# Optimization experiments

Hardware: AMD Instinct MI355X
Metric: run time of the kernel (lower is better)

## Reference

```python
import jax, jax.numpy as jnp
import numpy as np

B, N, C, PH, PW = 16, 256, 1, 16, 16
G, HID = 8, 256
TEMP = 0.5
EPS = 1e-5


def setup_inputs() -> dict:
    key = jax.random.key(0)
    ks = jax.random.split(key, 16)
    f32 = jnp.float32
    def kaiming(k, shape):  # fan_out mode for convs, OIHW
        fan_out = shape[0] * shape[2] * shape[3]
        return jax.random.normal(k, shape, f32) * np.float32(np.sqrt(2.0 / fan_out))
    def lin(k, shape):  # nn.init.normal_(w, 0, 0.01)
        return jax.random.normal(k, shape, f32) * np.float32(0.01)
    return {
        "x": jax.random.normal(ks[0], (B, N, C, PH, PW), f32),
        "conv1_w": kaiming(ks[1], (32, 1, 3, 3)),  "conv1_b": jnp.zeros((32,), f32),
        "bn1_g": jnp.ones((32,), f32),  "bn1_b": jnp.zeros((32,), f32),
        "conv2_w": kaiming(ks[2], (64, 32, 3, 3)), "conv2_b": jnp.zeros((64,), f32),
        "bn2_g": jnp.ones((64,), f32),  "bn2_b": jnp.zeros((64,), f32),
        "conv3_w": kaiming(ks[3], (128, 64, 3, 3)), "conv3_b": jnp.zeros((128,), f32),
        "bn3_g": jnp.ones((128,), f32), "bn3_b": jnp.zeros((128,), f32),
        "fc_w": lin(ks[4], (HID, 128)),       "fc_b": jnp.zeros((HID,), f32),
        "g1_w": lin(ks[5], (2 * HID, HID)),   "g1_b": jnp.zeros((2 * HID,), f32),
        "ln1_g": jnp.ones((2 * HID,), f32),   "ln1_b": jnp.zeros((2 * HID,), f32),
        "g2_w": lin(ks[6], (2 * HID, 2 * HID)), "g2_b": jnp.zeros((2 * HID,), f32),
        "ln2_g": jnp.ones((2 * HID,), f32),   "ln2_b": jnp.zeros((2 * HID,), f32),
        "g3_w": lin(ks[7], (G, 2 * HID)),     "g3_b": jnp.zeros((G,), f32),
    }


def _conv(h, w, b):
    out = jax.lax.conv_general_dilated(h, w, (1, 1), 'SAME',
        dimension_numbers=('NCHW', 'OIHW', 'NCHW'))
    return out + b[None, :, None, None]


def _bn_train(h, g, b):  # batch stats over (N, H, W), biased variance
    m = h.mean(axis=(0, 2, 3), keepdims=True)
    v = h.var(axis=(0, 2, 3), keepdims=True)
    return (h - m) * jax.lax.rsqrt(v + EPS) * g[None, :, None, None] + b[None, :, None, None]


def _ln(h, g, b):
    m = h.mean(axis=-1, keepdims=True)
    v = h.var(axis=-1, keepdims=True)
    return (h - m) * jax.lax.rsqrt(v + EPS) * g + b


def reference(x, conv1_w, conv1_b, bn1_g, bn1_b, conv2_w, conv2_b, bn2_g, bn2_b,
              conv3_w, conv3_b, bn3_g, bn3_b, fc_w, fc_b,
              g1_w, g1_b, ln1_g, ln1_b, g2_w, g2_b, ln2_g, ln2_b, g3_w, g3_b):
    Bx, Nx, Cx, ph, pw = x.shape
    Gx = g3_w.shape[0]
    K = Nx // Gx  # num_patches_per_group

    # ---- patch encoder (conv + BN(train) + ReLU x3, GAP, Linear) ----
    h = x.reshape(Bx * Nx, Cx, ph, pw)
    h = jax.nn.relu(_bn_train(_conv(h, conv1_w, conv1_b), bn1_g, bn1_b))
    h = jax.nn.relu(_bn_train(_conv(h, conv2_w, conv2_b), bn2_g, bn2_b))
    h = jax.nn.relu(_bn_train(_conv(h, conv3_w, conv3_b), bn3_g, bn3_b))
    feat = h.mean(axis=(2, 3))                     # [B*N, 128] (AdaptiveAvgPool2d(1))
    feat = feat @ fc_w.T + fc_b                    # [B*N, HID]
    feat = feat.reshape(Bx, Nx, -1)

    # ---- grouping network ----
    h = jax.nn.relu(_ln(feat @ g1_w.T + g1_b, ln1_g, ln1_b))
    h = jax.nn.relu(_ln(h @ g2_w.T + g2_b, ln2_g, ln2_b))
    logits = (h @ g3_w.T + g3_b) / TEMP            # [B, N, G]
    assignment = jax.nn.softmax(logits, axis=2)    # [B, N, G]

    # ---- per-group top-K weighted patch gather (training path) ----
    w = jnp.transpose(assignment, (0, 2, 1))       # [B, G, N]
    vals, idx = jax.lax.top_k(w, K)                # [B, G, K] (descending, matches sort)
    idx_e = idx[:, :, :, None, None, None]         # [B, G, K, 1, 1, 1]
    gathered = jnp.take_along_axis(x[:, None], idx_e, axis=2)  # [B, G, K, C, ph, pw]
    output = gathered * vals[:, :, :, None, None, None]
    return output, assignment
```

## Files before the change

kernel.cpp:

```cpp
#include <hip/hip_runtime.h>


#define WS_W1   0
#define WS_B1   288
#define WS_W2   320
#define WS_B2   18752
#define WS_W3   18816
#define WS_B3   92544
#define WS_FCW  92672
#define WS_FCB  125440
#define WS_G1W  125696
#define WS_G1B  256768
#define WS_L1G  257280
#define WS_L1B  257792
#define WS_G2W  258304
#define WS_G2B  520448
#define WS_L2G  520960
#define WS_L2B  521472
#define WS_G3W  521984
#define WS_G3B  526080
#define D_ACC1  263044
#define D_ACC2  (D_ACC1 + 4096)
#define D_ACC3  (D_ACC2 + 8192)
#define D_FEAT  (D_ACC3 + 16384)
#define D_AFF1  (D_FEAT + 524288)
#define D_AFF2  (D_AFF1 + 64)
#define D_AFF3  (D_AFF2 + 128)
#define D_ZN    553408
#define Z2_OFF_B 6532096ull


__global__ __launch_bounds__(256) void k_zero(double* __restrict__ dst){
  int i = blockIdx.x*256 + threadIdx.x;
  if(i < D_ZN) dst[i] = 0.0;
}

struct WP { const float* p[18]; };

__global__ __launch_bounds__(256) void k_cvt(WP wp, float* __restrict__ dst){
  const int segn[18] = {288,32,18432,64,73728,128,32768,256,131072,512,512,512,262144,512,512,512,4096,8};
  const int sego[18] = {WS_W1,WS_B1,WS_W2,WS_B2,WS_W3,WS_B3,WS_FCW,WS_FCB,WS_G1W,WS_G1B,
                        WS_L1G,WS_L1B,WS_G2W,WS_G2B,WS_L2G,WS_L2B,WS_G3W,WS_G3B};
  int s = blockIdx.y;
  int i = blockIdx.x*256 + threadIdx.x;
  if(i < segn[s]){
    if(s == 4){
      int oc = i / 576;
      int rem = i - oc*576;
      int ic = rem / 9;
      int j  = rem - ic*9;
      dst[WS_W3 + ic*1152 + j*128 + oc] = wp.p[4][i];
    } else {
      dst[sego[s]+i] = wp.p[s][i];
    }
  }
}

__global__ __launch_bounds__(64) void k_fin(const double* __restrict__ acc, int C,
                                            const float* __restrict__ gam, const float* __restrict__ bet,
                                            double* __restrict__ aff){
  int c = blockIdx.x, t = threadIdx.x;
  double s = acc[t*2*C + c*2];
  double q = acc[t*2*C + c*2 + 1];
  #pragma unroll
  for(int off=32;off;off>>=1){ s += __shfl_down(s,off); q += __shfl_down(q,off); }
  if(t==0){
    double m = s*(1.0/1048576.0);
    double v = q*(1.0/1048576.0) - m*m;
    double sc = (double)gam[c] / sqrt(v + 1e-5);
    aff[2*c]   = sc;
    aff[2*c+1] = (double)bet[c] - m*sc;
  }
}

__global__ __launch_bounds__(256) void k_p1(const float* __restrict__ x, const float* __restrict__ wf,
                                            double* __restrict__ acc1){
  __shared__ float xp[324];
  __shared__ double red[4][32][2];
  int p = blockIdx.x, t = threadIdx.x;
  for(int i=t;i<324;i+=256) xp[i]=0.f;
  __syncthreads();
  int py=t>>4, px=t&15;
  xp[(py+1)*18 + px + 1] = x[(size_t)p*256+t];
  __syncthreads();
  float nb[9];
  #pragma unroll
  for(int j=0;j<9;j++) nb[j] = xp[(py+j/3)*18 + px + (j%3)];
  int wave=t>>6, lane=t&63;
  for(int c=0;c<32;c++){
    float a = wf[WS_B1+c];
    #pragma unroll
    for(int j=0;j<9;j++) a = fmaf(nb[j], wf[WS_W1+c*9+j], a);
    double av=(double)a;
    double s=av, q=av*av;
    #pragma unroll
    for(int off=32;off;off>>=1){ s+=__shfl_down(s,off); q+=__shfl_down(q,off); }
    if(lane==0){ red[wave][c][0]=s; red[wave][c][1]=q; }
  }
  __syncthreads();
  if(t<64){
    int c=t>>1, st=t&1;
    double v = red[0][c][st]+red[1][c][st]+red[2][c][st]+red[3][c][st];
    atomicAdd(&acc1[(p&63)*64 + c*2 + st], v);
  }
}

__global__ __launch_bounds__(256) void k_p2(const float* __restrict__ x, const float* __restrict__ wf,
                                            const double* __restrict__ aff1, double* __restrict__ acc2,
                                            float* __restrict__ z2, int nS){
  __shared__ float xp[324];
  __shared__ float h1f[32*324];
  int p=blockIdx.x, t=threadIdx.x;
  for(int i=t;i<324;i+=256) xp[i]=0.f;
  for(int i=t;i<32*324;i+=256) h1f[i]=0.f;
  __syncthreads();
  int py=t>>4, px=t&15;
  xp[(py+1)*18 + px + 1] = x[(size_t)p*256+t];
  __syncthreads();
  {
    float nb[9];
    #pragma unroll
    for(int j=0;j<9;j++) nb[j] = xp[(py+j/3)*18 + px + (j%3)];
    for(int c=0;c<32;c++){
      float a = wf[WS_B1+c];
      #pragma unroll
      for(int j=0;j<9;j++) a = fmaf(nb[j], wf[WS_W1+c*9+j], a);
      h1f[c*324 + (py+1)*18 + (px+1)] = fmaxf(fmaf((float)aff1[2*c], a, (float)aff1[2*c+1]), 0.f);
    }
  }
  __syncthreads();
  int col=t&15, og=t>>4;
  bool wr = (p < nS);
  double sT[4]={0,0,0,0}, qT[4]={0,0,0,0};
  #pragma unroll 1
  for(int half=0; half<2; ++half){
    float acc[4][8];
    #pragma unroll
    for(int o=0;o<4;o++){
      float bv = wf[WS_B2 + og*4 + o];
      #pragma unroll
      for(int r=0;r<8;r++) acc[o][r]=bv;
    }
    #pragma unroll 1
    for(int ic=0; ic<32; ++ic){
      const float* wrow = wf + WS_W2 + (og*4*32 + ic)*9;
      #pragma unroll
      for(int j=0;j<9;j++){
        float w4[4];
        #pragma unroll
        for(int o=0;o<4;o++) w4[o] = wrow[o*288 + j];
        int dy=j/3, dx=j%3;
        #pragma unroll
        for(int r=0;r<8;r++){
          float m = h1f[ic*324 + (half*8 + r + dy)*18 + col + dx];
          #pragma unroll
          for(int o=0;o<4;o++) acc[o][r] = fmaf(m, w4[o], acc[o][r]);
        }
      }
    }
    #pragma unroll
    for(int o=0;o<4;o++){
      #pragma unroll
      for(int r=0;r<8;r++){ double v=(double)acc[o][r]; sT[o]+=v; qT[o]+=v*v; }
      if(wr){
        int c = og*4+o;
        #pragma unroll
        for(int r=0;r<8;r++) z2[((size_t)p*64+c)*256 + (half*8+r)*16 + col] = acc[o][r];
      }
    }
  }
  #pragma unroll
  for(int o=0;o<4;o++){
    double s=sT[o], q=qT[o];
    #pragma unroll
    for(int off=8;off;off>>=1){ s+=__shfl_down(s,off,16); q+=__shfl_down(q,off,16); }
    if(col==0){
      int c = og*4+o;
      atomicAdd(&acc2[(p&63)*128 + c*2 + 0], s);
      atomicAdd(&acc2[(p&63)*128 + c*2 + 1], q);
    }
  }
}

__global__ __launch_bounds__(512) void k_cs(const float* __restrict__ wf, const double* __restrict__ aff2,
                                            double* __restrict__ acc3, const float* __restrict__ z2){
  __shared__ float h2S[32*180];
  int bid=blockIdx.x, t=threadIdx.x;
  int p = bid>>1, r0 = (bid&1)*8;
  for(int i=t;i<5760;i+=512) h2S[i]=0.f;
  int col=t&15, og=t>>4;
  float acc[4][8];
  #pragma unroll
  for(int o=0;o<4;o++){
    float bv = wf[WS_B3 + og*4 + o];
    #pragma unroll
    for(int r=0;r<8;r++) acc[o][r]=bv;
  }
  const float* wog = wf + WS_W3 + og*4;
  float4 wc = *reinterpret_cast<const float4*>(wog);
  #pragma unroll 1
  for(int half=0; half<2; ++half){
    __syncthreads();
    for(int i=t;i<5120;i+=512){
      int ch2 = i/160, rem = i - ch2*160;
      int row = rem>>4, c2 = rem&15;
      int gr = r0 - 1 + row;
      if(gr>=0 && gr<16){
        int ch = half*32 + ch2;
        float zv = z2[((size_t)p*64+ch)*256 + gr*16 + c2];
        h2S[ch2*180 + row*18 + c2+1] = fmaxf(fmaf((float)aff2[2*ch], zv, (float)aff2[2*ch+1]), 0.f);
      }
    }
    __syncthreads();
    #pragma unroll 1
    for(int ic2=0; ic2<32; ++ic2){
      int ic = half*32 + ic2;
      float a[10][3];
      #pragma unroll
      for(int lr=0; lr<10; ++lr){
        #pragma unroll
        for(int dx=0; dx<3; ++dx) a[lr][dx] = h2S[ic2*180 + lr*18 + col + dx];
      }
      const float* wp = wog + ic*1152;
      #pragma unroll
      for(int j=0;j<9;j++){
        float4 wn = *reinterpret_cast<const float4*>(wp + (j+1)*128);
        int dy=j/3, dx=j%3;
        float w4[4] = {wc.x, wc.y, wc.z, wc.w};
        #pragma unroll
        for(int o=0;o<4;o++){
          #pragma unroll
          for(int r=0;r<8;r++) acc[o][r] = fmaf(a[r+dy][dx], w4[o], acc[o][r]);
        }
        wc = wn;
      }
    }
  }
  #pragma unroll
  for(int o=0;o<4;o++){
    double s=0.0, q=0.0;
    #pragma unroll
    for(int r=0;r<8;r++){ double v=(double)acc[o][r]; s+=v; q+=v*v; }
    #pragma unroll
    for(int off=8; off; off>>=1){ s += __shfl_down(s, off, 16); q += __shfl_down(q, off, 16); }
    if(col==0){
      int c = og*4+o;
      atomicAdd(&acc3[(bid&63)*256 + c*2 + 0], s);
      atomicAdd(&acc3[(bid&63)*256 + c*2 + 1], q);
    }
  }
}

__global__ __launch_bounds__(512) void k_cf(const float* __restrict__ wf, const double* __restrict__ aff2,
                                            const double* __restrict__ aff3, double* __restrict__ feat,
                                            const float* __restrict__ z2){
  __shared__ float h2S[32*180];
  int bid=blockIdx.x, t=threadIdx.x;
  int p = bid>>1, r0 = (bid&1)*8;
  for(int i=t;i<5760;i+=512) h2S[i]=0.f;
  int col=t&15, og=t>>4;
  float acc[4][8];
  #pragma unroll
  for(int o=0;o<4;o++){
    float bv = wf[WS_B3 + og*4 + o];
    #pragma unroll
    for(int r=0;r<8;r++) acc[o][r]=bv;
  }
  const float* wog = wf + WS_W3 + og*4;
  float4 wc = *reinterpret_cast<const float4*>(wog);
  #pragma unroll 1
  for(int half=0; half<2; ++half){
    __syncthreads();
    for(int i=t;i<5120;i+=512){
      int ch2 = i/160, rem = i - ch2*160;
      int row = rem>>4, c2 = rem&15;
      int gr = r0 - 1 + row;
      if(gr>=0 && gr<16){
        int ch = half*32 + ch2;
        float zv = z2[((size_t)p*64+ch)*256 + gr*16 + c2];
        h2S[ch2*180 + row*18 + c2+1] = fmaxf(fmaf((float)aff2[2*ch], zv, (float)aff2[2*ch+1]), 0.f);
      }
    }
    __syncthreads();
    #pragma unroll 1
    for(int ic2=0; ic2<32; ++ic2){
      int ic = half*32 + ic2;
      float a[10][3];
      #pragma unroll
      for(int lr=0; lr<10; ++lr){
        #pragma unroll
        for(int dx=0; dx<3; ++dx) a[lr][dx] = h2S[ic2*180 + lr*18 + col + dx];
      }
      const float* wp = wog + ic*1152;
      #pragma unroll
      for(int j=0;j<9;j++){
        float4 wn = *reinterpret_cast<const float4*>(wp + (j+1)*128);
        int dy=j/3, dx=j%3;
        float w4[4] = {wc.x, wc.y, wc.z, wc.w};
        #pragma unroll
        for(int o=0;o<4;o++){
          #pragma unroll
          for(int r=0;r<8;r++) acc[o][r] = fmaf(a[r+dy][dx], w4[o], acc[o][r]);
        }
        wc = wn;
      }
    }
  }
  #pragma unroll
  for(int o=0;o<4;o++){
    int c = og*4+o;
    float sc=(float)aff3[2*c], sh=(float)aff3[2*c+1];
    double sv = 0.0;
    #pragma unroll
    for(int r=0;r<8;r++) sv += (double)fmaxf(fmaf(sc, acc[o][r], sh), 0.f);
    #pragma unroll
    for(int off=8; off; off>>=1) sv += __shfl_down(sv, off, 16);
    if(col==0) atomicAdd(&feat[(size_t)p*128 + c], sv);
  }
}

__global__ __launch_bounds__(256) void k_stat3(const float* __restrict__ x, const float* __restrict__ wf,
                                               const double* __restrict__ aff1, const double* __restrict__ aff2,
                                               double* __restrict__ acc3, int p0){
  __shared__ float xp[324];
  __shared__ float h1S[32*144];
  __shared__ float h2S[64*108];
  int bid=blockIdx.x, t=threadIdx.x;
  int p = p0 + (bid>>2), r0 = (bid&3)*4;
  for(int i=t;i<64*108;i+=256) h2S[i]=0.f;
  for(int i=t;i<324;i+=256) xp[i]=0.f;
  for(int i=t;i<32*144;i+=256) h1S[i]=0.f;
  __syncthreads();
  { int py=t>>4, px=t&15; xp[(py+1)*18 + px + 1] = x[(size_t)p*256+t]; }
  __syncthreads();
  {
    int rr=t>>5, cw=t&31, col=cw&15, half=cw>>4;
    int p1 = r0-1+rr;
    if(p1>=1 && p1<=16){
      float nb[9];
      #pragma unroll
      for(int j=0;j<9;j++) nb[j] = xp[(p1-1+j/3)*18 + col + (j%3)];
      for(int k=0;k<16;k++){
        int c = half*16+k;
        float a = wf[WS_B1+c];
        #pragma unroll
        for(int j=0;j<9;j++) a = fmaf(nb[j], wf[WS_W1+c*9+j], a);
        h1S[c*144 + rr*18 + col+1] = fmaxf((float)aff1[2*c]*a + (float)aff1[2*c+1], 0.f);
      }
    }
  }
  __syncthreads();
  {
    int col=t&15, g=t>>4;
    float a24[4][6];
    #pragma unroll
    for(int o=0;o<4;o++){
      float bv = wf[WS_B2+g*4+o];
      #pragma unroll
      for(int b2=0;b2<6;b2++) a24[o][b2] = bv;
    }
    #pragma unroll 1
    for(int ic=0;ic<32;ic++){
      const float* wrow = wf + WS_W2 + (g*4*32 + ic)*9;
      #pragma unroll
      for(int j=0;j<9;j++){
        float w4[4];
        #pragma unroll
        for(int o=0;o<4;o++) w4[o] = wrow[o*288 + j];
        int dy=j/3, dx=j%3;
        #pragma unroll
        for(int b2=0;b2<6;b2++){
          float m = h1S[ic*144 + (b2+dy)*18 + col + dx];
          #pragma unroll
          for(int o=0;o<4;o++) a24[o][b2] = fmaf(m, w4[o], a24[o][b2]);
        }
      }
    }
    #pragma unroll
    for(int b2=0;b2<6;b2++){
      int p2 = r0+b2;
      if(p2>=1 && p2<=16){
        #pragma unroll
        for(int o=0;o<4;o++){
          int c=g*4+o;
          h2S[c*108 + b2*18 + col+1] = fmaxf((float)aff2[2*c]*a24[o][b2] + (float)aff2[2*c+1], 0.f);
        }
      }
    }
  }
  __syncthreads();
  {
    int col = t & 15, og = t >> 4;
    float acc[8][4];
    #pragma unroll
    for(int o=0;o<8;o++){
      float bv = wf[WS_B3 + og*8 + o];
      #pragma unroll
      for(int r=0;r<4;r++) acc[o][r] = bv;
    }
    #pragma unroll 1
    for(int ic=0; ic<64; ++ic){
      float a[6][3];
      #pragma unroll
      for(int rr=0; rr<6; ++rr){
        #pragma unroll
        for(int dx=0; dx<3; ++dx) a[rr][dx] = h2S[ic*108 + rr*18 + col + dx];
      }
      const float* wrow = wf + WS_W3 + ic*1152;
      #pragma unroll
      for(int o=0;o<8;o++){
        #pragma unroll
        for(int j=0;j<9;j++){
          float w = wrow[j*128 + og*8 + o];
          #pragma unroll
          for(int r=0;r<4;r++) acc[o][r] = fmaf(a[r + j/3][j%3], w, acc[o][r]);
        }
      }
    }
    #pragma unroll
    for(int o=0;o<8;o++){
      double s=0.0, q=0.0;
      #pragma unroll
      for(int r=0;r<4;r++){ double v=(double)acc[o][r]; s+=v; q+=v*v; }
      #pragma unroll
      for(int off=8; off; off>>=1){ s += __shfl_down(s, off, 16); q += __shfl_down(q, off, 16); }
      if(col==0){
        int c = og*8+o;
        atomicAdd(&acc3[(bid&63)*256 + c*2 + 0], s);
        atomicAdd(&acc3[(bid&63)*256 + c*2 + 1], q);
      }
    }
  }
}

__global__ __launch_bounds__(256) void k_p34(const float* __restrict__ x, const float* __restrict__ wf,
                                             const double* __restrict__ aff1, const double* __restrict__ aff2,
                                             const double* __restrict__ aff3, double* __restrict__ outp,
                                             int p0){
  __shared__ float xp[324];
  __shared__ float h1S[32*144];
  __shared__ float h2S[64*108];
  int bid=blockIdx.x, t=threadIdx.x;
  int p = p0 + (bid>>2), r0 = (bid&3)*4;
  for(int i=t;i<64*108;i+=256) h2S[i]=0.f;
  for(int i=t;i<324;i+=256) xp[i]=0.f;
  for(int i=t;i<32*144;i+=256) h1S[i]=0.f;
  __syncthreads();
  { int py=t>>4, px=t&15; xp[(py+1)*18 + px + 1] = x[(size_t)p*256+t]; }
  __syncthreads();
  {
    int rr=t>>5, cw=t&31, col=cw&15, half=cw>>4;
    int p1 = r0-1+rr;
    if(p1>=1 && p1<=16){
      float nb[9];
      #pragma unroll
      for(int j=0;j<9;j++) nb[j] = xp[(p1-1+j/3)*18 + col + (j%3)];
      for(int k=0;k<16;k++){
        int c = half*16+k;
        float a = wf[WS_B1+c];
        #pragma unroll
        for(int j=0;j<9;j++) a = fmaf(nb[j], wf[WS_W1+c*9+j], a);
        h1S[c*144 + rr*18 + col+1] = fmaxf((float)aff1[2*c]*a + (float)aff1[2*c+1], 0.f);
      }
    }
  }
  __syncthreads();
  {
    int col=t&15, g=t>>4;
    float a24[4][6];
    #pragma unroll
    for(int o=0;o<4;o++){
      float bv = wf[WS_B2+g*4+o];
      #pragma unroll
      for(int b2=0;b2<6;b2++) a24[o][b2] = bv;
    }
    #pragma unroll 1
    for(int ic=0;ic<32;ic++){
      const float* wrow = wf + WS_W2 + (g*4*32 + ic)*9;
      #pragma unroll
      for(int j=0;j<9;j++){
        float w4[4];
        #pragma unroll
        for(int o=0;o<4;o++) w4[o] = wrow[o*288 + j];
        int dy=j/3, dx=j%3;
        #pragma unroll
        for(int b2=0;b2<6;b2++){
          float m = h1S[ic*144 + (b2+dy)*18 + col + dx];
          #pragma unroll
          for(int o=0;o<4;o++) a24[o][b2] = fmaf(m, w4[o], a24[o][b2]);
        }
      }
    }
    #pragma unroll
    for(int b2=0;b2<6;b2++){
      int p2 = r0+b2;
      if(p2>=1 && p2<=16){
        #pragma unroll
        for(int o=0;o<4;o++){
          int c=g*4+o;
          h2S[c*108 + b2*18 + col+1] = fmaxf((float)aff2[2*c]*a24[o][b2] + (float)aff2[2*c+1], 0.f);
        }
      }
    }
  }
  __syncthreads();
  {
    int col = t & 15, og = t >> 4;
    float acc[8][4];
    #pragma unroll
    for(int o=0;o<8;o++){
      float bv = wf[WS_B3 + og*8 + o];
      #pragma unroll
      for(int r=0;r<4;r++) acc[o][r] = bv;
    }
    #pragma unroll 1
    for(int ic=0; ic<64; ++ic){
      float a[6][3];
      #pragma unroll
      for(int rr=0; rr<6; ++rr){
        #pragma unroll
        for(int dx=0; dx<3; ++dx) a[rr][dx] = h2S[ic*108 + rr*18 + col + dx];
      }
      const float* wrow = wf + WS_W3 + ic*1152;
      #pragma unroll
      for(int o=0;o<8;o++){
        #pragma unroll
        for(int j=0;j<9;j++){
          float w = wrow[j*128 + og*8 + o];
          #pragma unroll
          for(int r=0;r<4;r++) acc[o][r] = fmaf(a[r + j/3][j%3], w, acc[o][r]);
        }
      }
    }
    #pragma unroll
    for(int o=0;o<8;o++){
      int c = og*8+o;
      float sc=(float)aff3[2*c], sh=(float)aff3[2*c+1];
      double s = 0.0;
      #pragma unroll
      for(int r=0;r<4;r++) s += (double)fmaxf(fmaf(sc, acc[o][r], sh), 0.f);
      #pragma unroll
      for(int off=8; off; off>>=1) s += __shfl_down(s, off, 16);
      if(col==0) atomicAdd(&outp[(size_t)p*128 + c], s);
    }
  }
}

__device__ __forceinline__ void ln_relu4(double* buf, const float* __restrict__ g, const float* __restrict__ b,
                                         double* lnm, double* lnr, int t){
  int r=t>>6, j=t&63;
  double s=0.0, q=0.0;
  for(int k=j;k<512;k+=64){ double v=buf[r*512+k]; s+=v; q+=v*v; }
  #pragma unroll
  for(int off=32;off;off>>=1){ s+=__shfl_down(s,off); q+=__shfl_down(q,off); }
  if(j==0){
    double m = s*(1.0/512.0);
    double v = q*(1.0/512.0) - m*m;
    lnm[r]=m; lnr[r]=1.0/sqrt(v + 1e-5);
  }
  __syncthreads();
  for(int i=t;i<2048;i+=256){
    int r2=i>>9, k=i&511;
    double v=(buf[i]-lnm[r2])*lnr[r2]*(double)g[k]+(double)b[k];
    buf[i]=fmax(v,0.0);
  }
  __syncthreads();
}

__global__ __launch_bounds__(256) void k_mlp(const float* __restrict__ wf, const double* __restrict__ feat,
                                             float* __restrict__ assign_out){
  int r0 = blockIdx.x*4, t = threadIdx.x;
  __shared__ double f0[4*128];
  __shared__ double f1[4*256];
  __shared__ double f2[4*512];
  __shared__ double f3[4*512];
  __shared__ double lnm[4], lnr[4];
  __shared__ double lg[4][8];

  for(int i=t;i<512;i+=256) f0[i] = feat[(size_t)r0*128 + i] * (1.0/256.0);
  __syncthreads();
  {
    double acc[4];
    double bv = (double)wf[WS_FCB + t];
    #pragma unroll
    for(int r=0;r<4;r++) acc[r]=bv;
    for(int k=0;k<128;k++){
      double wv = (double)wf[WS_FCW + t*128 + k];
      #pragma unroll
      for(int r=0;r<4;r++) acc[r]=fma(wv, f0[r*128+k], acc[r]);
    }
    #pragma unroll
    for(int r=0;r<4;r++) f1[r*256+t]=acc[r];
  }
  __syncthreads();
  for(int half=0;half<2;half++){
    int i=t+(half<<8);
    double acc[4];
    double bv=(double)wf[WS_G1B+i];
    #pragma unroll
    for(int r=0;r<4;r++) acc[r]=bv;
    for(int k=0;k<256;k++){
      double wv=(double)wf[WS_G1W + i*256 + k];
      #pragma unroll
      for(int r=0;r<4;r++) acc[r]=fma(wv, f1[r*256+k], acc[r]);
    }
    #pragma unroll
    for(int r=0;r<4;r++) f2[r*512+i]=acc[r];
  }
  __syncthreads();
  ln_relu4(f2, wf+WS_L1G, wf+WS_L1B, lnm, lnr, t);
  for(int half=0;half<2;half++){
    int i=t+(half<<8);
    double acc[4];
    double bv=(double)wf[WS_G2B+i];
    #pragma unroll
    for(int r=0;r<4;r++) acc[r]=bv;
    for(int k=0;k<512;k++){
      double wv=(double)wf[WS_G2W + i*512 + k];
      #pragma unroll
      for(int r=0;r<4;r++) acc[r]=fma(wv, f2[r*512+k], acc[r]);
    }
    #pragma unroll
    for(int r=0;r<4;r++) f3[r*512+i]=acc[r];
  }
  __syncthreads();
  ln_relu4(f3, wf+WS_L2G, wf+WS_L2B, lnm, lnr, t);
  {
    int r=t>>6, j=t&63;
    double pl[8];
    #pragma unroll
    for(int g=0;g<8;g++){
      double s=0.0;
      for(int k=j;k<512;k+=64) s = fma(f3[r*512+k], (double)wf[WS_G3W + g*512 + k], s);
      pl[g]=s;
    }
    #pragma unroll
    for(int off=32;off;off>>=1){
      #pragma unroll
      for(int g=0;g<8;g++) pl[g] += __shfl_down(pl[g], off);
    }
    if(j==0){
      #pragma unroll
      for(int g=0;g<8;g++) lg[r][g] = (pl[g] + (double)wf[WS_G3B+g]) * 2.0;
    }
  }
  __syncthreads();
  if(t<4){
    double m=-1e300;
    #pragma unroll
    for(int g=0;g<8;g++) m = fmax(m, lg[t][g]);
    double e[8], s=0.0;
    #pragma unroll
    for(int g=0;g<8;g++){ e[g]=exp(lg[t][g]-m); s+=e[g]; }
    double inv = 1.0/s;
    int row = r0 + t;
    #pragma unroll
    for(int g=0;g<8;g++) assign_out[row*8+g] = (float)(e[g]*inv);
  }
}

__global__ __launch_bounds__(256) void k_topk(const float* __restrict__ assign, const float* __restrict__ x,
                                              float* __restrict__ out){
  int b = blockIdx.x >> 3, g = blockIdx.x & 7, t = threadIdx.x;
  __shared__ float v[256];
  __shared__ int   id[256];
  v[t] = assign[(b*256+t)*8 + g];
  id[t] = t;
  __syncthreads();
  for(int k=2;k<=256;k<<=1){
    for(int j=k>>1;j>0;j>>=1){
      int ixj = t ^ j;
      if(ixj > t){
        float va=v[t], vb=v[ixj];
        int ia=id[t], ib=id[ixj];
        bool aBefore = (va > vb) || (va == vb && ia < ib);
        bool up = ((t & k) == 0);
        if(up != aBefore){ v[t]=vb; v[ixj]=va; id[t]=ib; id[ixj]=ia; }
      }
      __syncthreads();
    }
  }
  __shared__ float tv[32];
  __shared__ int   ti[32];
  if(t<32){ tv[t]=v[t]; ti[t]=id[t]; }
  __syncthreads();
  const float* xb = x + (size_t)b*65536;
  float* ob = out + (size_t)(b*8+g)*8192;
  for(int i=t;i<8192;i+=256){
    int k=i>>8, pix=i&255;
    ob[i] = tv[k] * xb[ti[k]*256 + pix];
  }
}

extern "C" void kernel_launch(void* const* d_in, const int* in_sizes, int n_in,
                              void* d_out, int out_size, void* d_ws, size_t ws_size,
                              hipStream_t stream){
  const float* x = (const float*)d_in[0];
  float*  ws  = (float*)d_ws;
  double* dws = (double*)d_ws;
  float* out = (float*)d_out;
  float* assign_out = out + 1048576;
  float* z2 = (float*)((char*)d_ws + Z2_OFF_B);

  int nS = 0;
  if(ws_size > Z2_OFF_B + 65536){
    unsigned long long avail = (unsigned long long)ws_size - Z2_OFF_B;
    unsigned long long n = avail / 65536ull;
    nS = (n > 4096ull) ? 4096 : (int)n;
  }
  int nR = 4096 - nS;

  const float* g1=(const float*)d_in[3];  const float* b1=(const float*)d_in[4];
  const float* g2=(const float*)d_in[7];  const float* b2=(const float*)d_in[8];
  const float* g3=(const float*)d_in[11]; const float* b3=(const float*)d_in[12];

  WP wp;
  const int map[18] = {1,2,5,6,9,10,13,14,15,16,17,18,19,20,21,22,23,24};
  for(int i=0;i<18;i++) wp.p[i] = (const float*)d_in[map[i]];

  k_zero <<<2162, 256, 0, stream>>>(dws + D_ACC1);
  k_cvt  <<<dim3(1024,18), 256, 0, stream>>>(wp, ws);
  k_p1   <<<4096, 256, 0, stream>>>(x, ws, dws+D_ACC1);
  k_fin  <<<32, 64, 0, stream>>>(dws+D_ACC1, 32, g1, b1, dws+D_AFF1);
  k_p2   <<<4096, 256, 0, stream>>>(x, ws, dws+D_AFF1, dws+D_ACC2, z2, nS);
  k_fin  <<<64, 64, 0, stream>>>(dws+D_ACC2, 64, g2, b2, dws+D_AFF2);
  if(nS > 0) k_cs   <<<2*nS, 512, 0, stream>>>(ws, dws+D_AFF2, dws+D_ACC3, z2);
  if(nR > 0) k_stat3<<<4*nR, 256, 0, stream>>>(x, ws, dws+D_AFF1, dws+D_AFF2, dws+D_ACC3, nS);
  k_fin  <<<128, 64, 0, stream>>>(dws+D_ACC3, 128, g3, b3, dws+D_AFF3);
  if(nS > 0) k_cf  <<<2*nS, 512, 0, stream>>>(ws, dws+D_AFF2, dws+D_AFF3, dws+D_FEAT, z2);
  if(nR > 0) k_p34 <<<4*nR, 256, 0, stream>>>(x, ws, dws+D_AFF1, dws+D_AFF2, dws+D_AFF3, dws+D_FEAT, nS);
  k_mlp  <<<1024, 256, 0, stream>>>(ws, dws+D_FEAT, assign_out);
  k_topk <<<128, 256, 0, stream>>>(assign_out, x, out);
}
```

Before: 4.898 ms.

## Retile conv3 kernels so each wave owns 16 output channels with uniform weights

Changes the thread-to-output mapping in the conv3 stats and feature kernels. Each 64-lane wave now computes 16 output channels for 2 rows per lane, instead of each 16-lane group handling 4 channels for 8 rows. Weights become wave-uniform, so they can come through scalar loads as a 16-float vector, and fewer shared-memory reads are needed per input channel. The shared tile row stride is padded from 18 to 20 floats, and reductions now run across the full wave. The trade-off is less input reuse per weight (2 rows instead of 8), which raises the FMA-to-LDS-read ratio per element.

```diff
diff --git a/kernel.cpp b/kernel.cpp
--- a/kernel.cpp
+++ b/kernel.cpp
@@ -1,5 +1,7 @@
 #include <hip/hip_runtime.h>
 
+
+typedef float f32x16 __attribute__((ext_vector_type(16)));
 
 #define WS_W1   0
 #define WS_B1   288
@@ -184,20 +186,19 @@
 
 __global__ __launch_bounds__(512) void k_cs(const float* __restrict__ wf, const double* __restrict__ aff2,
                                             double* __restrict__ acc3, const float* __restrict__ z2){
-  __shared__ float h2S[32*180];
+  __shared__ float h2S[32*200];
   int bid=blockIdx.x, t=threadIdx.x;
   int p = bid>>1, r0 = (bid&1)*8;
-  for(int i=t;i<5760;i+=512) h2S[i]=0.f;
-  int col=t&15, og=t>>4;
-  float acc[4][8];
+  for(int i=t;i<6400;i+=512) h2S[i]=0.f;
+  int col=t&15, q=(t>>4)&3;
+  int wv = __builtin_amdgcn_readfirstlane(t>>6);
+  float acc[16][2];
   #pragma unroll
-  for(int o=0;o<4;o++){
-    float bv = wf[WS_B3 + og*4 + o];
-    #pragma unroll
-    for(int r=0;r<8;r++) acc[o][r]=bv;
-  }
-  const float* wog = wf + WS_W3 + og*4;
-  float4 wc = *reinterpret_cast<const float4*>(wog);
+  for(int o=0;o<16;o++){
+    float bv = wf[WS_B3 + wv*16 + o];
+    acc[o][0]=bv; acc[o][1]=bv;
+  }
+  const f32x16* wW = reinterpret_cast<const f32x16*>(wf + WS_W3 + wv*16);
   #pragma unroll 1
   for(int half=0; half<2; ++half){
     __syncthreads();
@@ -208,45 +209,41 @@
       if(gr>=0 && gr<16){
         int ch = half*32 + ch2;
         float zv = z2[((size_t)p*64+ch)*256 + gr*16 + c2];
-        h2S[ch2*180 + row*18 + c2+1] = fmaxf(fmaf((float)aff2[2*ch], zv, (float)aff2[2*ch+1]), 0.f);
+        h2S[ch2*200 + row*20 + c2+1] = fmaxf(fmaf((float)aff2[2*ch], zv, (float)aff2[2*ch+1]), 0.f);
       }
     }
     __syncthreads();
     #pragma unroll 1
     for(int ic2=0; ic2<32; ++ic2){
       int ic = half*32 + ic2;
-      float a[10][3];
-      #pragma unroll
-      for(int lr=0; lr<10; ++lr){
-        #pragma unroll
-        for(int dx=0; dx<3; ++dx) a[lr][dx] = h2S[ic2*180 + lr*18 + col + dx];
-      }
-      const float* wp = wog + ic*1152;
+      float a[4][3];
+      #pragma unroll
+      for(int lr=0; lr<4; ++lr){
+        #pragma unroll
+        for(int dx=0; dx<3; ++dx) a[lr][dx] = h2S[ic2*200 + (2*q+lr)*20 + col + dx];
+      }
       #pragma unroll
       for(int j=0;j<9;j++){
-        float4 wn = *reinterpret_cast<const float4*>(wp + (j+1)*128);
+        f32x16 w = wW[ic*72 + j*8];
         int dy=j/3, dx=j%3;
-        float w4[4] = {wc.x, wc.y, wc.z, wc.w};
-        #pragma unroll
-        for(int o=0;o<4;o++){
-          #pragma unroll
-          for(int r=0;r<8;r++) acc[o][r] = fmaf(a[r+dy][dx], w4[o], acc[o][r]);
-        }
-        wc = wn;
+        #pragma unroll
+        for(int o=0;o<16;o++){
+          acc[o][0] = fmaf(a[dy  ][dx], w[o], acc[o][0]);
+          acc[o][1] = fmaf(a[dy+1][dx], w[o], acc[o][1]);
+        }
       }
     }
   }
   #pragma unroll
-  for(int o=0;o<4;o++){
-    double s=0.0, q=0.0;
-    #pragma unroll
-    for(int r=0;r<8;r++){ double v=(double)acc[o][r]; s+=v; q+=v*v; }
-    #pragma unroll
-    for(int off=8; off; off>>=1){ s += __shfl_down(s, off, 16); q += __shfl_down(q, off, 16); }
-    if(col==0){
-      int c = og*4+o;
+  for(int o=0;o<16;o++){
+    double s  = (double)acc[o][0] + (double)acc[o][1];
+    double q2 = (double)acc[o][0]*(double)acc[o][0] + (double)acc[o][1]*(double)acc[o][1];
+    #pragma unroll
+    for(int off=32;off;off>>=1){ s += __shfl_down(s,off); q2 += __shfl_down(q2,off); }
+    if((t&63)==0){
+      int c = wv*16+o;
       atomicAdd(&acc3[(bid&63)*256 + c*2 + 0], s);
-      atomicAdd(&acc3[(bid&63)*256 + c*2 + 1], q);
+      atomicAdd(&acc3[(bid&63)*256 + c*2 + 1], q2);
     }
   }
 }
@@ -254,20 +251,19 @@
 __global__ __launch_bounds__(512) void k_cf(const float* __restrict__ wf, const double* __restrict__ aff2,
                                             const double* __restrict__ aff3, double* __restrict__ feat,
                                             const float* __restrict__ z2){
-  __shared__ float h2S[32*180];
+  __shared__ float h2S[32*200];
   int bid=blockIdx.x, t=threadIdx.x;
   int p = bid>>1, r0 = (bid&1)*8;
-  for(int i=t;i<5760;i+=512) h2S[i]=0.f;
-  int col=t&15, og=t>>4;
-  float acc[4][8];
+  for(int i=t;i<6400;i+=512) h2S[i]=0.f;
+  int col=t&15, q=(t>>4)&3;
+  int wv = __builtin_amdgcn_readfirstlane(t>>6);
+  float acc[16][2];
   #pragma unroll
-  for(int o=0;o<4;o++){
-    float bv = wf[WS_B3 + og*4 + o];
-    #pragma unroll
-    for(int r=0;r<8;r++) acc[o][r]=bv;
-  }
-  const float* wog = wf + WS_W3 + og*4;
-  float4 wc = *reinterpret_cast<const float4*>(wog);
+  for(int o=0;o<16;o++){
+    float bv = wf[WS_B3 + wv*16 + o];
+    acc[o][0]=bv; acc[o][1]=bv;
+  }
+  const f32x16* wW = reinterpret_cast<const f32x16*>(wf + WS_W3 + wv*16);
   #pragma unroll 1
   for(int half=0; half<2; ++half){
     __syncthreads();
@@ -278,44 +274,40 @@
       if(gr>=0 && gr<16){
         int ch = half*32 + ch2;
         float zv = z2[((size_t)p*64+ch)*256 + gr*16 + c2];
-        h2S[ch2*180 + row*18 + c2+1] = fmaxf(fmaf((float)aff2[2*ch], zv, (float)aff2[2*ch+1]), 0.f);
+        h2S[ch2*200 + row*20 + c2+1] = fmaxf(fmaf((float)aff2[2*ch], zv, (float)aff2[2*ch+1]), 0.f);
       }
     }
     __syncthreads();
     #pragma unroll 1
     for(int ic2=0; ic2<32; ++ic2){
       int ic = half*32 + ic2;
-      float a[10][3];
-      #pragma unroll
-      for(int lr=0; lr<10; ++lr){
-        #pragma unroll
-        for(int dx=0; dx<3; ++dx) a[lr][dx] = h2S[ic2*180 + lr*18 + col + dx];
-      }
-      const float* wp = wog + ic*1152;
+      float a[4][3];
+      #pragma unroll
+      for(int lr=0; lr<4; ++lr){
+        #pragma unroll
+        for(int dx=0; dx<3; ++dx) a[lr][dx] = h2S[ic2*200 + (2*q+lr)*20 + col + dx];
+      }
       #pragma unroll
       for(int j=0;j<9;j++){
-        float4 wn = *reinterpret_cast<const float4*>(wp + (j+1)*128);
+        f32x16 w = wW[ic*72 + j*8];
         int dy=j/3, dx=j%3;
-        float w4[4] = {wc.x, wc.y, wc.z, wc.w};
-        #pragma unroll
-        for(int o=0;o<4;o++){
-          #pragma unroll
-          for(int r=0;r<8;r++) acc[o][r] = fmaf(a[r+dy][dx], w4[o], acc[o][r]);
-        }
-        wc = wn;
+        #pragma unroll
+        for(int o=0;o<16;o++){
+          acc[o][0] = fmaf(a[dy  ][dx], w[o], acc[o][0]);
+          acc[o][1] = fmaf(a[dy+1][dx], w[o], acc[o][1]);
+        }
       }
     }
   }
   #pragma unroll
-  for(int o=0;o<4;o++){
-    int c = og*4+o;
+  for(int o=0;o<16;o++){
+    int c = wv*16+o;
     float sc=(float)aff3[2*c], sh=(float)aff3[2*c+1];
-    double sv = 0.0;
-    #pragma unroll
-    for(int r=0;r<8;r++) sv += (double)fmaxf(fmaf(sc, acc[o][r], sh), 0.f);
-    #pragma unroll
-    for(int off=8; off; off>>=1) sv += __shfl_down(sv, off, 16);
-    if(col==0) atomicAdd(&feat[(size_t)p*128 + c], sv);
+    double sv = (double)fmaxf(fmaf(sc, acc[o][0], sh), 0.f)
+              + (double)fmaxf(fmaf(sc, acc[o][1], sh), 0.f);
+    #pragma unroll
+    for(int off=32;off;off>>=1) sv += __shfl_down(sv,off);
+    if((t&63)==0) atomicAdd(&feat[(size_t)p*128 + c], sv);
   }
 }
 
```

New measurement: 4.040 ms. 17.5% less time.
